# Performance work log

Measured on AMD Instinct MI355X. Metric: run time of the kernel, lower is better.

## Reference

```python
import jax, jax.numpy as jnp
import numpy as np

N = 100_000      # nodes
E = 800_000      # edges
NF = 32          # node_feature_size
EF = 32          # edge_feature_size
L = 64           # layer_size
ENTRY = NF + EF          # 64, input width of node_mlp_1
SECOND = NF + L          # 96, input width of node_mlp_2
SLOPE = 0.1              # leakiness
EPS = 1e-5               # BatchNorm1d eps


def _bn(h, g, b):
    # BatchNorm1d in training mode: batch mean, biased variance
    m = h.mean(0)
    v = ((h - m) ** 2).mean(0)
    return (h - m) * jax.lax.rsqrt(v + EPS) * g + b


def _lrelu(h):
    return jnp.where(h > 0, h, SLOPE * h)


def setup_inputs() -> dict:
    key = jax.random.key(0)
    ks = jax.random.split(key, 16)

    def w(k, i, o):
        return (jax.random.normal(k, (i, o), jnp.float32) / np.float32(np.sqrt(i)))

    def bvec(k, o):
        return jax.random.normal(k, (o,), jnp.float32) * 0.01

    inp = {
        "x": jax.random.normal(ks[0], (N, NF), jnp.float32),
        "edge_index": jax.random.randint(ks[1], (2, E), 0, N),
        "edge_attr": jax.random.normal(ks[2], (E, EF), jnp.float32),
        "u": jax.random.normal(ks[3], (1, 4), jnp.float32),
        "batch": jnp.zeros((N,), jnp.int32),
        # node_mlp_1 params
        "m1_g1": jnp.ones((ENTRY,), jnp.float32), "m1_b1": jnp.zeros((ENTRY,), jnp.float32),
        "m1_w1": w(ks[4], ENTRY, L), "m1_c1": bvec(ks[5], L),
        "m1_g2": jnp.ones((L,), jnp.float32), "m1_b2": jnp.zeros((L,), jnp.float32),
        "m1_w2": w(ks[6], L, L), "m1_c2": bvec(ks[7], L),
        "m1_g3": jnp.ones((L,), jnp.float32), "m1_b3": jnp.zeros((L,), jnp.float32),
        "m1_w3": w(ks[8], L, L), "m1_c3": bvec(ks[9], L),
        # node_mlp_2 params
        "m2_g1": jnp.ones((SECOND,), jnp.float32), "m2_b1": jnp.zeros((SECOND,), jnp.float32),
        "m2_w1": w(ks[10], SECOND, SECOND), "m2_c1": bvec(ks[11], SECOND),
        "m2_g2": jnp.ones((SECOND,), jnp.float32), "m2_b2": jnp.zeros((SECOND,), jnp.float32),
        "m2_w2": w(ks[12], SECOND, SECOND), "m2_c2": bvec(ks[13], SECOND),
        "m2_g3": jnp.ones((SECOND,), jnp.float32), "m2_b3": jnp.zeros((SECOND,), jnp.float32),
        "m2_w3": w(ks[14], SECOND, NF), "m2_c3": bvec(ks[15], NF),
    }
    return inp


def reference(x, edge_index, edge_attr, u, batch,
              m1_g1, m1_b1, m1_w1, m1_c1,
              m1_g2, m1_b2, m1_w2, m1_c2,
              m1_g3, m1_b3, m1_w3, m1_c3,
              m2_g1, m2_b1, m2_w1, m2_c1,
              m2_g2, m2_b2, m2_w2, m2_c2,
              m2_g3, m2_b3, m2_w3, m2_c3):
    row, col = edge_index[0], edge_index[1]
    # gather source node features, concat with edge features  [E, ENTRY]
    h = jnp.concatenate([x[row], edge_attr], axis=1)
    # node_mlp_1: BN -> Linear -> LReLU -> BN -> Linear -> LReLU -> BN -> Linear
    h = _lrelu(_bn(h, m1_g1, m1_b1) @ m1_w1 + m1_c1)
    h = _lrelu(_bn(h, m1_g2, m1_b2) @ m1_w2 + m1_c2)
    h = _bn(h, m1_g3, m1_b3) @ m1_w3 + m1_c3
    # scatter-sum back to destination nodes  [N, L]
    agg = jax.ops.segment_sum(h, col, num_segments=x.shape[0])
    # node_mlp_2 on [x, agg]  [N, SECOND]
    h2 = jnp.concatenate([x, agg], axis=1)
    h2 = _lrelu(_bn(h2, m2_g1, m2_b1) @ m2_w1 + m2_c1)
    h2 = _lrelu(_bn(h2, m2_g2, m2_b2) @ m2_w2 + m2_c2)
    out = _bn(h2, m2_g3, m2_b3) @ m2_w3 + m2_c3  # [N, NF]
    return out
```

## Files before the change

### kernel.cpp

```cpp
#include <hip/hip_runtime.h>


typedef unsigned short u16;
typedef __bf16  bf16x8  __attribute__((ext_vector_type(8)));
typedef float   floatx4 __attribute__((ext_vector_type(4)));

#define NBIN 8

__device__ __forceinline__ float bf2f(u16 u) {
  union { float f; unsigned int i; } v; v.i = ((unsigned int)u) << 16; return v.f;
}
__device__ __forceinline__ u16 f2bf(float f) {
  union { float f; unsigned int i; } v; v.f = f;
  unsigned int x = v.i;
  return (u16)((x + 0x7fffu + ((x >> 16) & 1u)) >> 16);
}
__device__ __forceinline__ bf16x8 ldb8(const u16* p) {
  return *reinterpret_cast<const bf16x8*>(p);
}
__device__ __forceinline__ floatx4 mfma16(bf16x8 a, bf16x8 b, floatx4 c) {
  return __builtin_amdgcn_mfma_f32_16x16x32_bf16(a, b, c, 0, 0, 0);
}
__device__ __forceinline__ float loadf(const void* p, long idx, int mode) {
  return mode ? bf2f(((const u16*)p)[idx]) : ((const float*)p)[idx];
}
__device__ __forceinline__ bf16x8 load8(const void* p, long idx, int mode) {
  if (mode) return ldb8((const u16*)p + idx);
  const float* f = (const float*)p + idx;
  bf16x8 r;
#pragma unroll
  for (int j = 0; j < 8; j++) r[j] = (__bf16)f[j];
  return r;
}

__global__ void detect_kernel(const u16* __restrict__ x, int* __restrict__ modep) {
  __shared__ int cnt;
  if (threadIdx.x == 0) cnt = 0;
  __syncthreads();
  int weird = 0;
  for (int i = threadIdx.x; i < 1024; i += blockDim.x) {
    unsigned e = (x[i] >> 7) & 0xFFu;
    if (e == 0xFFu || e >= 0x90u || (e != 0u && e < 0x60u)) weird++;
  }
  atomicAdd(&cnt, weird);
  __syncthreads();
  if (threadIdx.x == 0) *modep = (cnt > 128) ? 0 : 1;
}

__global__ void count2_kernel(const int* __restrict__ row, const int* __restrict__ col,
                              int E, int* __restrict__ odeg, int* __restrict__ deg) {
  for (int e = blockIdx.x * blockDim.x + threadIdx.x; e < E;
       e += gridDim.x * blockDim.x) {
    atomicAdd(&odeg[row[e]], 1);
    atomicAdd(&deg[col[e]], 1);
  }
}

__global__ void scan1_kernel(const int* __restrict__ deg, int n,
                             int* __restrict__ excl, int* __restrict__ bsum) {
  __shared__ int tmp[2][1024];
  const int tid = threadIdx.x;
  const int i = blockIdx.x * 1024 + tid;
  int v = (i < n) ? deg[i] : 0;
  tmp[0][tid] = v;
  __syncthreads();
  int src = 0;
  for (int off = 1; off < 1024; off <<= 1) {
    int t = tmp[src][tid];
    if (tid >= off) t += tmp[src][tid - off];
    tmp[1 - src][tid] = t;
    src = 1 - src;
    __syncthreads();
  }
  if (i < n) excl[i] = tmp[src][tid] - v;
  if (tid == 1023) bsum[blockIdx.x] = tmp[src][1023];
}

__global__ void scan2_kernel(int* __restrict__ bsum, int nb,
                             int* __restrict__ offsets, int N, int E) {
  if (threadIdx.x == 0) {
    int run = 0;
    for (int i = 0; i < nb; i++) { int v = bsum[i]; bsum[i] = run; run += v; }
    offsets[N] = E;
  }
}

__global__ void scan3_kernel(int* __restrict__ offsets, const int* __restrict__ bsum,
                             int n, int* __restrict__ cursor) {
  int i = blockIdx.x * 1024 + threadIdx.x;
  if (i < n) {
    int v = offsets[i] + bsum[blockIdx.x];
    offsets[i] = v;
    cursor[i] = v;
  }
}

__global__ void scatter_kernel(const int* __restrict__ col, int E,
                               int* __restrict__ cursor, int* __restrict__ ipos) {
  for (int e = blockIdx.x * blockDim.x + threadIdx.x; e < E;
       e += gridDim.x * blockDim.x) {
    int d = col[e];
    ipos[e] = atomicAdd(&cursor[d], 1);
  }
}

__global__ void statsXW_kernel(const void* __restrict__ x, const int* __restrict__ odeg,
                               int N, float* __restrict__ stats0,
                               float* __restrict__ statsB0,
                               const int* __restrict__ modep) {
  const int mode = *modep;
  const int c = threadIdx.x & 31, rs = threadIdx.x >> 5;
  float s = 0.f, q = 0.f, ws = 0.f, wq = 0.f;
  for (long r = (long)blockIdx.x * 8 + rs; r < N; r += (long)gridDim.x * 8) {
    float v = loadf(x, r * 32 + c, mode);
    float w = (float)odeg[r];
    s += v; q += v * v;
    ws += w * v; wq += w * v * v;
  }
  __shared__ float sm[4][256];
  sm[0][threadIdx.x] = s; sm[1][threadIdx.x] = q;
  sm[2][threadIdx.x] = ws; sm[3][threadIdx.x] = wq;
  __syncthreads();
  if (threadIdx.x < 32) {
    for (int i = 1; i < 8; i++) {
      s  += sm[0][i * 32 + c]; q  += sm[1][i * 32 + c];
      ws += sm[2][i * 32 + c]; wq += sm[3][i * 32 + c];
    }
    const int bin = blockIdx.x & (NBIN - 1);
    atomicAdd(statsB0 + bin * 192 + c, s);
    atomicAdd(statsB0 + bin * 192 + 96 + c, q);
    atomicAdd(stats0 + bin * 128 + c, ws);
    atomicAdd(stats0 + bin * 128 + 64 + c, wq);
  }
}

__global__ void statsEA_kernel(const void* __restrict__ ea, int E,
                               float* __restrict__ stats,
                               const int* __restrict__ modep) {
  const int mode = *modep;
  const int cg = threadIdx.x & 3;
  const int rsub = threadIdx.x >> 2;
  float s[8], q[8];
#pragma unroll
  for (int j = 0; j < 8; j++) { s[j] = 0.f; q[j] = 0.f; }
  for (long r = (long)blockIdx.x * 64 + rsub; r < E; r += (long)gridDim.x * 64) {
    if (mode) {
      bf16x8 v = ldb8((const u16*)ea + r * 32 + cg * 8);
#pragma unroll
      for (int j = 0; j < 8; j++) { float f = (float)v[j]; s[j] += f; q[j] += f * f; }
    } else {
      const float* p = (const float*)ea + r * 32 + cg * 8;
      float4 a = *(const float4*)p;
      float4 b = *(const float4*)(p + 4);
      float f0[8] = {a.x, a.y, a.z, a.w, b.x, b.y, b.z, b.w};
#pragma unroll
      for (int j = 0; j < 8; j++) { s[j] += f0[j]; q[j] += f0[j] * f0[j]; }
    }
  }
  const int lane = threadIdx.x & 63;
#pragma unroll
  for (int st = 4; st < 64; st <<= 1) {
#pragma unroll
    for (int j = 0; j < 8; j++) {
      s[j] += __shfl_xor(s[j], st, 64);
      q[j] += __shfl_xor(q[j], st, 64);
    }
  }
  if (lane < 4) {
    float* o = stats + (blockIdx.x & (NBIN - 1)) * 128;
#pragma unroll
    for (int j = 0; j < 8; j++) {
      atomicAdd(o + 32 + lane * 8 + j, s[j]);
      atomicAdd(o + 96 + lane * 8 + j, q[j]);
    }
  }
}

__global__ __launch_bounds__(256) void aggsum_kernel(
    const u16* __restrict__ h_s, const int* __restrict__ offsets,
    float* __restrict__ s_e, int N) {
  const int lane = threadIdx.x & 63, wave = threadIdx.x >> 6;
  for (long n = (long)blockIdx.x * 4 + wave; n < N; n += (long)gridDim.x * 4) {
    int start = offsets[n], end = offsets[n + 1];
    float acc = 0.f;
    for (int j = start; j < end; j++)
      acc += bf2f(h_s[(long)j * 64 + lane]);
    s_e[n * 64 + lane] = acc;
  }
}

__global__ void fold_kernel(const float* __restrict__ stats, float inv_rows,
                            const void* __restrict__ g, const void* __restrict__ b,
                            const void* __restrict__ W, const void* __restrict__ c,
                            int K, int OUT,
                            u16* __restrict__ Wpack, float* __restrict__ biasOut,
                            const int* __restrict__ modep) {
  const int mode = *modep;
  __shared__ float s_s[96], s_off[96];
  const int tid = threadIdx.x;
  if (tid < K) {
    float sum = 0.f, sq = 0.f;
    for (int p = 0; p < NBIN; p++) {
      sum += stats[p * 2 * K + tid];
      sq  += stats[p * 2 * K + K + tid];
    }
    float m   = sum * inv_rows;
    float var = sq * inv_rows - m * m;
    float s   = loadf(g, tid, mode) * rsqrtf(var + 1e-5f);
    s_s[tid]  = s;
    s_off[tid] = loadf(b, tid, mode) - m * s;
  }
  __syncthreads();
  for (int n = tid; n < OUT; n += blockDim.x) {
    float acc = loadf(c, n, mode);
    for (int k = 0; k < K; k++) acc += s_off[k] * loadf(W, k * OUT + n, mode);
    biasOut[n] = acc;
  }
  const int H = K / 32, T = OUT / 16;
  const int total = T * H * 64 * 8;
  for (int i = tid; i < total; i += blockDim.x) {
    int j = i & 7, lane = (i >> 3) & 63, th = i >> 9;
    int h = th % H, t = th / H;
    int k = h * 32 + (lane >> 4) * 8 + j;
    int n = t * 16 + (lane & 15);
    Wpack[i] = f2bf(s_s[k] * loadf(W, k * OUT + n, mode));
  }
}


__global__ __launch_bounds__(256) void gemm1_kernel(
    const void* __restrict__ x, const void* __restrict__ ea,
    const int* __restrict__ erow, const int* __restrict__ ipos,
    const u16* __restrict__ Wp, const float* __restrict__ bias,
    u16* __restrict__ hout, int E,
    float* __restrict__ statsOut, const int* __restrict__ modep) {
  const int mode = *modep;
  const int lane = threadIdx.x & 63, wave = threadIdx.x >> 6;
  const int q = lane >> 4, r = lane & 15;
  const long wbase = (long)blockIdx.x * 256 + wave * 64;
  bf16x8 bfr[4][2];
#pragma unroll
  for (int t = 0; t < 4; t++)
#pragma unroll
    for (int h = 0; h < 2; h++)
      bfr[t][h] = ldb8(Wp + ((t * 2 + h) * 64 + lane) * 8);
  float bv[4];
#pragma unroll
  for (int t = 0; t < 4; t++) bv[t] = bias[t * 16 + r];
  float s_[4] = {0, 0, 0, 0}, q_[4] = {0, 0, 0, 0};
#pragma unroll
  for (int r4 = 0; r4 < 4; r4++) {
    const long row0 = wbase + r4 * 16;
    long e = row0 + r; if (e > E - 1) e = E - 1;
    int src = erow[e];
    bf16x8 a0 = load8(x, (long)src * 32 + q * 8, mode);
    bf16x8 a1 = load8(ea, e * 32 + q * 8, mode);
    floatx4 acc[4];
#pragma unroll
    for (int t = 0; t < 4; t++) {
      acc[t] = (floatx4){bv[t], bv[t], bv[t], bv[t]};
      acc[t] = mfma16(a0, bfr[t][0], acc[t]);
      acc[t] = mfma16(a1, bfr[t][1], acc[t]);
    }
#pragma unroll
    for (int gi = 0; gi < 4; gi++) {
      long row = row0 + q * 4 + gi;
      if (row < E) {
        long p = ipos[row];
#pragma unroll
        for (int t = 0; t < 4; t++) {
          float v = acc[t][gi];
          v = v > 0.f ? v : 0.1f * v;
          u16 st = f2bf(v);
          hout[p * 64 + t * 16 + r] = st;
          float vv = bf2f(st);
          s_[t] += vv; q_[t] += vv * vv;
        }
      }
    }
  }
  __shared__ float sm[512];
#pragma unroll
  for (int t = 0; t < 4; t++) {
    float s = s_[t], qq = q_[t];
    s  += __shfl_xor(s, 16, 64);  s  += __shfl_xor(s, 32, 64);
    qq += __shfl_xor(qq, 16, 64); qq += __shfl_xor(qq, 32, 64);
    if (lane < 16) { sm[wave * 128 + t * 16 + lane] = s; sm[wave * 128 + 64 + t * 16 + lane] = qq; }
  }
  __syncthreads();
  if (threadIdx.x < 128) {
    int which = threadIdx.x >> 6, c = threadIdx.x & 63;
    float v = 0.f;
    for (int w = 0; w < 4; w++) v += sm[w * 128 + which * 64 + c];
    atomicAdd(statsOut + (blockIdx.x & (NBIN - 1)) * 128 + which * 64 + c, v);
  }
}

__global__ __launch_bounds__(256) void gemm2_kernel(
    const u16* __restrict__ hin, const u16* __restrict__ Wp,
    const float* __restrict__ bias, u16* __restrict__ hout, int E,
    float* __restrict__ statsOut) {
  const int lane = threadIdx.x & 63, wave = threadIdx.x >> 6;
  const int q = lane >> 4, r = lane & 15;
  const long wbase = (long)blockIdx.x * 256 + wave * 64;
  bf16x8 bfr[4][2];
#pragma unroll
  for (int t = 0; t < 4; t++)
#pragma unroll
    for (int h = 0; h < 2; h++)
      bfr[t][h] = ldb8(Wp + ((t * 2 + h) * 64 + lane) * 8);
  float bv[4];
#pragma unroll
  for (int t = 0; t < 4; t++) bv[t] = bias[t * 16 + r];
  float s_[4] = {0, 0, 0, 0}, q_[4] = {0, 0, 0, 0};
#pragma unroll
  for (int r4 = 0; r4 < 4; r4++) {
    const long row0 = wbase + r4 * 16;
    long e = row0 + r; if (e > E - 1) e = E - 1;
    bf16x8 a0 = ldb8(hin + e * 64 + q * 8);
    bf16x8 a1 = ldb8(hin + e * 64 + 32 + q * 8);
    floatx4 acc[4];
#pragma unroll
    for (int t = 0; t < 4; t++) {
      acc[t] = (floatx4){bv[t], bv[t], bv[t], bv[t]};
      acc[t] = mfma16(a0, bfr[t][0], acc[t]);
      acc[t] = mfma16(a1, bfr[t][1], acc[t]);
    }
#pragma unroll
    for (int t = 0; t < 4; t++)
#pragma unroll
      for (int gi = 0; gi < 4; gi++) {
        long row = row0 + q * 4 + gi;
        if (row < E) {
          float v = acc[t][gi];
          v = v > 0.f ? v : 0.1f * v;
          u16 st = f2bf(v);
          hout[row * 64 + t * 16 + r] = st;
          float vv = bf2f(st);
          s_[t] += vv; q_[t] += vv * vv;
        }
      }
  }
  __shared__ float sm[512];
#pragma unroll
  for (int t = 0; t < 4; t++) {
    float s = s_[t], qq = q_[t];
    s  += __shfl_xor(s, 16, 64);  s  += __shfl_xor(s, 32, 64);
    qq += __shfl_xor(qq, 16, 64); qq += __shfl_xor(qq, 32, 64);
    if (lane < 16) { sm[wave * 128 + t * 16 + lane] = s; sm[wave * 128 + 64 + t * 16 + lane] = qq; }
  }
  __syncthreads();
  if (threadIdx.x < 128) {
    int which = threadIdx.x >> 6, c = threadIdx.x & 63;
    float v = 0.f;
    for (int w = 0; w < 4; w++) v += sm[w * 128 + which * 64 + c];
    atomicAdd(statsOut + (blockIdx.x & (NBIN - 1)) * 128 + which * 64 + c, v);
  }
}

__global__ __launch_bounds__(256) void gemmAgg_kernel(
    const float* __restrict__ s_e, const int* __restrict__ deg,
    const u16* __restrict__ Wp, const float* __restrict__ bias,
    float* __restrict__ agg, int N, float* __restrict__ statsOut) {
  const int lane = threadIdx.x & 63, wave = threadIdx.x >> 6;
  const int q = lane >> 4, r = lane & 15;
  const long wbase = (long)blockIdx.x * 256 + wave * 64;
  bf16x8 bfr[4][2];
#pragma unroll
  for (int t = 0; t < 4; t++)
#pragma unroll
    for (int h = 0; h < 2; h++)
      bfr[t][h] = ldb8(Wp + ((t * 2 + h) * 64 + lane) * 8);
  float bv[4];
#pragma unroll
  for (int t = 0; t < 4; t++) bv[t] = bias[t * 16 + r];
  float s_[4] = {0, 0, 0, 0}, q_[4] = {0, 0, 0, 0};
#pragma unroll
  for (int r4 = 0; r4 < 4; r4++) {
    const long row0 = wbase + r4 * 16;
    long m = row0 + r;
    long mm = m < N ? m : (long)N - 1;
    bf16x8 a0, a1;
    {
      const float* ap = s_e + mm * 64 + q * 8;
#pragma unroll
      for (int j = 0; j < 8; j++) a0[j] = (__bf16)ap[j];
#pragma unroll
      for (int j = 0; j < 8; j++) a1[j] = (__bf16)ap[32 + j];
    }
    floatx4 acc[4];
#pragma unroll
    for (int t = 0; t < 4; t++) {
      acc[t] = (floatx4){0.f, 0.f, 0.f, 0.f};
      acc[t] = mfma16(a0, bfr[t][0], acc[t]);
      acc[t] = mfma16(a1, bfr[t][1], acc[t]);
    }
#pragma unroll
    for (int gi = 0; gi < 4; gi++) {
      long row = row0 + q * 4 + gi;
      if (row < N) {
        float d = (float)deg[row];
#pragma unroll
        for (int t = 0; t < 4; t++) {
          float v = acc[t][gi] + d * bv[t];
          agg[row * 64 + t * 16 + r] = v;
          s_[t] += v; q_[t] += v * v;
        }
      }
    }
  }
  __shared__ float sm[512];
#pragma unroll
  for (int t = 0; t < 4; t++) {
    float s = s_[t], qq = q_[t];
    s  += __shfl_xor(s, 16, 64);  s  += __shfl_xor(s, 32, 64);
    qq += __shfl_xor(qq, 16, 64); qq += __shfl_xor(qq, 32, 64);
    if (lane < 16) { sm[wave * 128 + t * 16 + lane] = s; sm[wave * 128 + 64 + t * 16 + lane] = qq; }
  }
  __syncthreads();
  if (threadIdx.x < 128) {
    int which = threadIdx.x >> 6, c = threadIdx.x & 63;
    float v = 0.f;
    for (int w = 0; w < 4; w++) v += sm[w * 128 + which * 64 + c];
    atomicAdd(statsOut + (blockIdx.x & (NBIN - 1)) * 192 + which * 96 + 32 + c, v);
  }
}


__global__ __launch_bounds__(256) void gemmB1_kernel(
    const void* __restrict__ x, const float* __restrict__ agg,
    const u16* __restrict__ Wp, const float* __restrict__ bias,
    u16* __restrict__ hout, int N, float* __restrict__ statsOut,
    const int* __restrict__ modep) {
  const int mode = *modep;
  const int lane = threadIdx.x & 63, wave = threadIdx.x >> 6;
  const int q = lane >> 4, r = lane & 15;
  const long wbase = (long)blockIdx.x * 256 + wave * 64;
  bf16x8 bfr[6][3];
#pragma unroll
  for (int t = 0; t < 6; t++)
#pragma unroll
    for (int h = 0; h < 3; h++)
      bfr[t][h] = ldb8(Wp + ((t * 3 + h) * 64 + lane) * 8);
  float bv[6];
#pragma unroll
  for (int t = 0; t < 6; t++) bv[t] = bias[t * 16 + r];
  float s_[6] = {0, 0, 0, 0, 0, 0}, q_[6] = {0, 0, 0, 0, 0, 0};
#pragma unroll
  for (int r4 = 0; r4 < 4; r4++) {
    const long row0 = wbase + r4 * 16;
    long m = row0 + r;
    long mm = m < N ? m : (long)N - 1;
    bf16x8 a0 = load8(x, mm * 32 + q * 8, mode);
    bf16x8 a1, a2;
    {
      const float* ap = agg + mm * 64 + q * 8;
#pragma unroll
      for (int j = 0; j < 8; j++) a1[j] = (__bf16)ap[j];
#pragma unroll
      for (int j = 0; j < 8; j++) a2[j] = (__bf16)ap[32 + j];
    }
    floatx4 acc[6];
#pragma unroll
    for (int t = 0; t < 6; t++) {
      acc[t] = (floatx4){bv[t], bv[t], bv[t], bv[t]};
      acc[t] = mfma16(a0, bfr[t][0], acc[t]);
      acc[t] = mfma16(a1, bfr[t][1], acc[t]);
      acc[t] = mfma16(a2, bfr[t][2], acc[t]);
    }
#pragma unroll
    for (int t = 0; t < 6; t++)
#pragma unroll
      for (int gi = 0; gi < 4; gi++) {
        long row = row0 + q * 4 + gi;
        if (row < N) {
          float v = acc[t][gi];
          v = v > 0.f ? v : 0.1f * v;
          u16 st = f2bf(v);
          hout[row * 96 + t * 16 + r] = st;
          float vv = bf2f(st);
          s_[t] += vv; q_[t] += vv * vv;
        }
      }
  }
  __shared__ float sm[768];
#pragma unroll
  for (int t = 0; t < 6; t++) {
    float s = s_[t], qq = q_[t];
    s  += __shfl_xor(s, 16, 64);  s  += __shfl_xor(s, 32, 64);
    qq += __shfl_xor(qq, 16, 64); qq += __shfl_xor(qq, 32, 64);
    if (lane < 16) { sm[wave * 192 + t * 16 + lane] = s; sm[wave * 192 + 96 + t * 16 + lane] = qq; }
  }
  __syncthreads();
  if (threadIdx.x < 192) {
    int which = threadIdx.x / 96, c = threadIdx.x % 96;
    float v = 0.f;
    for (int w = 0; w < 4; w++) v += sm[w * 192 + which * 96 + c];
    atomicAdd(statsOut + (blockIdx.x & (NBIN - 1)) * 192 + which * 96 + c, v);
  }
}

__global__ __launch_bounds__(256) void gemmB2_kernel(
    const u16* __restrict__ hin, const u16* __restrict__ Wp,
    const float* __restrict__ bias, u16* __restrict__ hout, int N,
    float* __restrict__ statsOut) {
  const int lane = threadIdx.x & 63, wave = threadIdx.x >> 6;
  const int q = lane >> 4, r = lane & 15;
  const long wbase = (long)blockIdx.x * 256 + wave * 64;
  bf16x8 bfr[6][3];
#pragma unroll
  for (int t = 0; t < 6; t++)
#pragma unroll
    for (int h = 0; h < 3; h++)
      bfr[t][h] = ldb8(Wp + ((t * 3 + h) * 64 + lane) * 8);
  float bv[6];
#pragma unroll
  for (int t = 0; t < 6; t++) bv[t] = bias[t * 16 + r];
  float s_[6] = {0, 0, 0, 0, 0, 0}, q_[6] = {0, 0, 0, 0, 0, 0};
#pragma unroll
  for (int r4 = 0; r4 < 4; r4++) {
    const long row0 = wbase + r4 * 16;
    long m = row0 + r;
    long mm = m < N ? m : (long)N - 1;
    bf16x8 a0 = ldb8(hin + mm * 96 + q * 8);
    bf16x8 a1 = ldb8(hin + mm * 96 + 32 + q * 8);
    bf16x8 a2 = ldb8(hin + mm * 96 + 64 + q * 8);
    floatx4 acc[6];
#pragma unroll
    for (int t = 0; t < 6; t++) {
      acc[t] = (floatx4){bv[t], bv[t], bv[t], bv[t]};
      acc[t] = mfma16(a0, bfr[t][0], acc[t]);
      acc[t] = mfma16(a1, bfr[t][1], acc[t]);
      acc[t] = mfma16(a2, bfr[t][2], acc[t]);
    }
#pragma unroll
    for (int t = 0; t < 6; t++)
#pragma unroll
      for (int gi = 0; gi < 4; gi++) {
        long row = row0 + q * 4 + gi;
        if (row < N) {
          float v = acc[t][gi];
          v = v > 0.f ? v : 0.1f * v;
          u16 st = f2bf(v);
          hout[row * 96 + t * 16 + r] = st;
          float vv = bf2f(st);
          s_[t] += vv; q_[t] += vv * vv;
        }
      }
  }
  __shared__ float sm[768];
#pragma unroll
  for (int t = 0; t < 6; t++) {
    float s = s_[t], qq = q_[t];
    s  += __shfl_xor(s, 16, 64);  s  += __shfl_xor(s, 32, 64);
    qq += __shfl_xor(qq, 16, 64); qq += __shfl_xor(qq, 32, 64);
    if (lane < 16) { sm[wave * 192 + t * 16 + lane] = s; sm[wave * 192 + 96 + t * 16 + lane] = qq; }
  }
  __syncthreads();
  if (threadIdx.x < 192) {
    int which = threadIdx.x / 96, c = threadIdx.x % 96;
    float v = 0.f;
    for (int w = 0; w < 4; w++) v += sm[w * 192 + which * 96 + c];
    atomicAdd(statsOut + (blockIdx.x & (NBIN - 1)) * 192 + which * 96 + c, v);
  }
}

__global__ __launch_bounds__(256) void gemmB3_kernel(
    const u16* __restrict__ hin, const u16* __restrict__ Wp,
    const float* __restrict__ bias, void* __restrict__ outv, int N,
    const int* __restrict__ modep) {
  const int mode = *modep;
  const int lane = threadIdx.x & 63, wave = threadIdx.x >> 6;
  const int q = lane >> 4, r = lane & 15;
  const long wbase = (long)blockIdx.x * 256 + wave * 64;
  bf16x8 bfr[2][3];
#pragma unroll
  for (int t = 0; t < 2; t++)
#pragma unroll
    for (int h = 0; h < 3; h++)
      bfr[t][h] = ldb8(Wp + ((t * 3 + h) * 64 + lane) * 8);
  float bv[2];
#pragma unroll
  for (int t = 0; t < 2; t++) bv[t] = bias[t * 16 + r];
#pragma unroll
  for (int r4 = 0; r4 < 4; r4++) {
    const long row0 = wbase + r4 * 16;
    long m = row0 + r;
    long mm = m < N ? m : (long)N - 1;
    bf16x8 a0 = ldb8(hin + mm * 96 + q * 8);
    bf16x8 a1 = ldb8(hin + mm * 96 + 32 + q * 8);
    bf16x8 a2 = ldb8(hin + mm * 96 + 64 + q * 8);
    floatx4 acc[2];
#pragma unroll
    for (int t = 0; t < 2; t++) {
      acc[t] = (floatx4){bv[t], bv[t], bv[t], bv[t]};
      acc[t] = mfma16(a0, bfr[t][0], acc[t]);
      acc[t] = mfma16(a1, bfr[t][1], acc[t]);
      acc[t] = mfma16(a2, bfr[t][2], acc[t]);
    }
#pragma unroll
    for (int t = 0; t < 2; t++)
#pragma unroll
      for (int gi = 0; gi < 4; gi++) {
        long row = row0 + q * 4 + gi;
        if (row < N) {
          float v = acc[t][gi];
          if (mode) ((u16*)outv)[row * 32 + t * 16 + r] = f2bf(v);
          else      ((float*)outv)[row * 32 + t * 16 + r] = v;
        }
      }
  }
}

extern "C" void kernel_launch(void* const* d_in, const int* in_sizes, int n_in,
                              void* d_out, int out_size, void* d_ws,
                              size_t ws_size, hipStream_t stream) {
  const int N = in_sizes[0] / 32;
  const int E = in_sizes[2] / 32;

  const void* x    = d_in[0];
  const int*  eidx = (const int*)d_in[1];
  const void* ea   = d_in[2];
  const void *m1_g1 = d_in[5],  *m1_b1 = d_in[6];
  const void *m1_w1 = d_in[7],  *m1_c1 = d_in[8];
  const void *m1_g2 = d_in[9],  *m1_b2 = d_in[10];
  const void *m1_w2 = d_in[11], *m1_c2 = d_in[12];
  const void *m1_g3 = d_in[13], *m1_b3 = d_in[14];
  const void *m1_w3 = d_in[15], *m1_c3 = d_in[16];
  const void *m2_g1 = d_in[17], *m2_b1 = d_in[18];
  const void *m2_w1 = d_in[19], *m2_c1 = d_in[20];
  const void *m2_g2 = d_in[21], *m2_b2 = d_in[22];
  const void *m2_w2 = d_in[23], *m2_c2 = d_in[24];
  const void *m2_g3 = d_in[25], *m2_b3 = d_in[26];
  const void *m2_w3 = d_in[27], *m2_c3 = d_in[28];

  char* w = (char*)d_ws;
  int*   modep  = (int*)w;   w += 16;
  u16*   h_s    = (u16*)w;   w += (size_t)E * 64 * 2;
  u16*   h2b    = (u16*)w;   w += (size_t)N * 96 * 2;
  float* agg    = (float*)w; w += (size_t)N * 64 * 4;
  float* s_e    = (float*)w; w += (size_t)N * 64 * 4;
  int*   offs   = (int*)w;   w += ((size_t)N + 4) * 4;
  int*   cursor = (int*)w;   w += ((size_t)N + 4) * 4;
  int*   ipos   = (int*)w;   w += (size_t)E * 4;
  int*   bsum   = (int*)w;   w += 1024 * 4;
  int*   deg    = (int*)w;   w += (size_t)N * 4;
  int*   odeg   = (int*)w;   w += (size_t)N * 4;
  float* stats0 = (float*)w; w += NBIN * 128 * 4;
  float* stats1 = (float*)w; w += NBIN * 128 * 4;
  float* stats2 = (float*)w; w += NBIN * 128 * 4;
  float* statsB0= (float*)w; w += NBIN * 192 * 4;
  float* statsB1= (float*)w; w += NBIN * 192 * 4;
  float* statsB2= (float*)w; w += NBIN * 192 * 4;
  const size_t zero_bytes = (size_t)N * 8 + NBIN * (128 * 3 + 192 * 3) * 4;
  u16*   Wp1    = (u16*)w;   w += 4096 * 2;
  float* bias1  = (float*)w; w += 64 * 4;
  u16*   Wp2    = (u16*)w;   w += 4096 * 2;
  float* bias2  = (float*)w; w += 64 * 4;
  u16*   Wp3    = (u16*)w;   w += 4096 * 2;
  float* bias3  = (float*)w; w += 64 * 4;
  u16*   WpB1   = (u16*)w;   w += 9216 * 2;
  float* biasB1 = (float*)w; w += 96 * 4;
  u16*   WpB2   = (u16*)w;   w += 9216 * 2;
  float* biasB2 = (float*)w; w += 96 * 4;
  u16*   WpB3   = (u16*)w;   w += 3072 * 2;
  float* biasB3 = (float*)w; w += 32 * 4;

  const int* erow = eidx;
  const int* ecol = eidx + E;
  const float invE = 1.0f / (float)E, invN = 1.0f / (float)N;
  const int gA = (E + 255) / 256, gB = (N + 255) / 256;
  const int nb = (N + 1023) / 1024;

  detect_kernel<<<1, 256, 0, stream>>>((const u16*)x, modep);
  hipMemsetAsync(deg, 0, zero_bytes, stream);

  count2_kernel<<<1024, 256, 0, stream>>>(erow, ecol, E, odeg, deg);
  scan1_kernel<<<nb, 1024, 0, stream>>>(deg, N, offs, bsum);
  scan2_kernel<<<1, 64, 0, stream>>>(bsum, nb, offs, N, E);
  scan3_kernel<<<nb, 1024, 0, stream>>>(offs, bsum, N, cursor);
  scatter_kernel<<<1024, 256, 0, stream>>>(ecol, E, cursor, ipos);

  statsXW_kernel<<<512, 256, 0, stream>>>(x, odeg, N, stats0, statsB0, modep);
  statsEA_kernel<<<512, 256, 0, stream>>>(ea, E, stats0, modep);

  fold_kernel<<<1, 256, 0, stream>>>(stats0, invE, m1_g1, m1_b1, m1_w1, m1_c1,
                                     64, 64, Wp1, bias1, modep);
  gemm1_kernel<<<gA, 256, 0, stream>>>(x, ea, erow, ipos, Wp1, bias1, h_s, E,
                                       stats1, modep);
  fold_kernel<<<1, 256, 0, stream>>>(stats1, invE, m1_g2, m1_b2, m1_w2, m1_c2,
                                     64, 64, Wp2, bias2, modep);
  gemm2_kernel<<<gA, 256, 0, stream>>>(h_s, Wp2, bias2, h_s, E, stats2);

  aggsum_kernel<<<1024, 256, 0, stream>>>(h_s, offs, s_e, N);
  fold_kernel<<<1, 256, 0, stream>>>(stats2, invE, m1_g3, m1_b3, m1_w3, m1_c3,
                                     64, 64, Wp3, bias3, modep);
  gemmAgg_kernel<<<gB, 256, 0, stream>>>(s_e, deg, Wp3, bias3, agg, N, statsB0);

  fold_kernel<<<1, 256, 0, stream>>>(statsB0, invN, m2_g1, m2_b1, m2_w1, m2_c1,
                                     96, 96, WpB1, biasB1, modep);
  gemmB1_kernel<<<gB, 256, 0, stream>>>(x, agg, WpB1, biasB1, h2b, N,
                                        statsB1, modep);
  fold_kernel<<<1, 256, 0, stream>>>(statsB1, invN, m2_g2, m2_b2, m2_w2, m2_c2,
                                     96, 96, WpB2, biasB2, modep);
  gemmB2_kernel<<<gB, 256, 0, stream>>>(h2b, WpB2, biasB2, h2b, N, statsB2);
  fold_kernel<<<1, 256, 0, stream>>>(statsB2, invN, m2_g3, m2_b3, m2_w3, m2_c3,
                                     96, 32, WpB3, biasB3, modep);
  gemmB3_kernel<<<gB, 256, 0, stream>>>(h2b, WpB3, biasB3, d_out, N, modep);
}
```

Baseline: 741.5 us.

## Fuse segment-sum aggregation into gemm2 via LDS tile and node map

gemm2 no longer writes its 800K x 64 bf16 output to global memory. It stages the tile in a swizzled LDS buffer and then sums rows per destination node inside the block, using a new nodeof array built in the scatter kernel. Segments that cross block boundaries are combined with atomics into a now zero-initialised s_e. This removes the separate aggsum kernel and a full round trip of h_s through global memory. In exchange it adds 32 KB of LDS per block, the extra nodeof writes, and a larger memset. fold_kernel also stages W in shared memory.

```diff
diff --git a/kernel.cpp b/kernel.cpp
--- a/kernel.cpp
+++ b/kernel.cpp
@@ -96,11 +96,14 @@
 }
 
 __global__ void scatter_kernel(const int* __restrict__ col, int E,
-                               int* __restrict__ cursor, int* __restrict__ ipos) {
+                               int* __restrict__ cursor, int* __restrict__ ipos,
+                               int* __restrict__ nodeof) {
   for (int e = blockIdx.x * blockDim.x + threadIdx.x; e < E;
        e += gridDim.x * blockDim.x) {
     int d = col[e];
-    ipos[e] = atomicAdd(&cursor[d], 1);
+    int pos = atomicAdd(&cursor[d], 1);
+    ipos[e] = pos;
+    nodeof[pos] = d;
   }
 }
 
@@ -176,19 +179,6 @@
   }
 }
 
-__global__ __launch_bounds__(256) void aggsum_kernel(
-    const u16* __restrict__ h_s, const int* __restrict__ offsets,
-    float* __restrict__ s_e, int N) {
-  const int lane = threadIdx.x & 63, wave = threadIdx.x >> 6;
-  for (long n = (long)blockIdx.x * 4 + wave; n < N; n += (long)gridDim.x * 4) {
-    int start = offsets[n], end = offsets[n + 1];
-    float acc = 0.f;
-    for (int j = start; j < end; j++)
-      acc += bf2f(h_s[(long)j * 64 + lane]);
-    s_e[n * 64 + lane] = acc;
-  }
-}
-
 __global__ void fold_kernel(const float* __restrict__ stats, float inv_rows,
                             const void* __restrict__ g, const void* __restrict__ b,
                             const void* __restrict__ W, const void* __restrict__ c,
@@ -197,7 +187,10 @@
                             const int* __restrict__ modep) {
   const int mode = *modep;
   __shared__ float s_s[96], s_off[96];
+  __shared__ float wlds[9216];
   const int tid = threadIdx.x;
+  const int tot = K * OUT;
+  for (int i = tid; i < tot; i += blockDim.x) wlds[i] = loadf(W, i, mode);
   if (tid < K) {
     float sum = 0.f, sq = 0.f;
     for (int p = 0; p < NBIN; p++) {
@@ -213,7 +206,7 @@
   __syncthreads();
   for (int n = tid; n < OUT; n += blockDim.x) {
     float acc = loadf(c, n, mode);
-    for (int k = 0; k < K; k++) acc += s_off[k] * loadf(W, k * OUT + n, mode);
+    for (int k = 0; k < K; k++) acc += s_off[k] * wlds[k * OUT + n];
     biasOut[n] = acc;
   }
   const int H = K / 32, T = OUT / 16;
@@ -223,7 +216,7 @@
     int h = th % H, t = th / H;
     int k = h * 32 + (lane >> 4) * 8 + j;
     int n = t * 16 + (lane & 15);
-    Wpack[i] = f2bf(s_s[k] * loadf(W, k * OUT + n, mode));
+    Wpack[i] = f2bf(s_s[k] * wlds[k * OUT + n]);
   }
 }
 
@@ -298,11 +291,16 @@
 
 __global__ __launch_bounds__(256) void gemm2_kernel(
     const u16* __restrict__ hin, const u16* __restrict__ Wp,
-    const float* __restrict__ bias, u16* __restrict__ hout, int E,
-    float* __restrict__ statsOut) {
+    const float* __restrict__ bias, int E,
+    float* __restrict__ statsOut,
+    const int* __restrict__ offs, const int* __restrict__ nodeof,
+    float* __restrict__ s_e) {
   const int lane = threadIdx.x & 63, wave = threadIdx.x >> 6;
   const int q = lane >> 4, r = lane & 15;
-  const long wbase = (long)blockIdx.x * 256 + wave * 64;
+  const long bbase = (long)blockIdx.x * 256;
+  const long wbase = bbase + wave * 64;
+  __shared__ u16 hs[256 * 64];
+  __shared__ float sm[512];
   bf16x8 bfr[4][2];
 #pragma unroll
   for (int t = 0; t < 4; t++)
@@ -326,22 +324,24 @@
       acc[t] = mfma16(a0, bfr[t][0], acc[t]);
       acc[t] = mfma16(a1, bfr[t][1], acc[t]);
     }
-#pragma unroll
-    for (int t = 0; t < 4; t++)
+    const int lbase = wave * 64 + r4 * 16;
+#pragma unroll
+    for (int t = 0; t < 4; t++) {
+      const int colx = ((t ^ q) << 4) + r;
 #pragma unroll
       for (int gi = 0; gi < 4; gi++) {
         long row = row0 + q * 4 + gi;
+        float v = acc[t][gi];
+        v = v > 0.f ? v : 0.1f * v;
+        u16 st = f2bf(v);
+        hs[(lbase + q * 4 + gi) * 64 + colx] = st;
         if (row < E) {
-          float v = acc[t][gi];
-          v = v > 0.f ? v : 0.1f * v;
-          u16 st = f2bf(v);
-          hout[row * 64 + t * 16 + r] = st;
           float vv = bf2f(st);
           s_[t] += vv; q_[t] += vv * vv;
         }
       }
-  }
-  __shared__ float sm[512];
+    }
+  }
 #pragma unroll
   for (int t = 0; t < 4; t++) {
     float s = s_[t], qq = q_[t];
@@ -355,6 +355,22 @@
     float v = 0.f;
     for (int w = 0; w < 4; w++) v += sm[w * 128 + which * 64 + c];
     atomicAdd(statsOut + (blockIdx.x & (NBIN - 1)) * 128 + which * 64 + c, v);
+  }
+  const long blockEnd = (bbase + 256 < (long)E) ? bbase + 256 : (long)E;
+  const int first = nodeof[bbase];
+  const int last  = nodeof[blockEnd - 1];
+  for (int idx = first + wave; idx <= last; idx += 4) {
+    int st = offs[idx], en = offs[idx + 1];
+    long cs = st < bbase ? bbase : (long)st;
+    long ce = (long)en > blockEnd ? blockEnd : (long)en;
+    if (cs >= ce) continue;
+    float acc = 0.f;
+    for (long i = cs - bbase; i < ce - bbase; i++)
+      acc += bf2f(hs[i * 64 + (lane ^ (int)(((i >> 2) & 3) << 4))]);
+    if ((long)st >= bbase && (long)en <= blockEnd)
+      s_e[(long)idx * 64 + lane] = acc;
+    else
+      atomicAdd(s_e + (long)idx * 64 + lane, acc);
   }
 }
 
@@ -639,11 +655,12 @@
   u16*   h_s    = (u16*)w;   w += (size_t)E * 64 * 2;
   u16*   h2b    = (u16*)w;   w += (size_t)N * 96 * 2;
   float* agg    = (float*)w; w += (size_t)N * 64 * 4;
-  float* s_e    = (float*)w; w += (size_t)N * 64 * 4;
   int*   offs   = (int*)w;   w += ((size_t)N + 4) * 4;
   int*   cursor = (int*)w;   w += ((size_t)N + 4) * 4;
   int*   ipos   = (int*)w;   w += (size_t)E * 4;
+  int*   nodeof = (int*)w;   w += (size_t)E * 4;
   int*   bsum   = (int*)w;   w += 1024 * 4;
+  float* s_e    = (float*)w; w += (size_t)N * 64 * 4;
   int*   deg    = (int*)w;   w += (size_t)N * 4;
   int*   odeg   = (int*)w;   w += (size_t)N * 4;
   float* stats0 = (float*)w; w += NBIN * 128 * 4;
@@ -652,7 +669,8 @@
   float* statsB0= (float*)w; w += NBIN * 192 * 4;
   float* statsB1= (float*)w; w += NBIN * 192 * 4;
   float* statsB2= (float*)w; w += NBIN * 192 * 4;
-  const size_t zero_bytes = (size_t)N * 8 + NBIN * (128 * 3 + 192 * 3) * 4;
+  const size_t zero_bytes = (size_t)N * 64 * 4 + (size_t)N * 8 +
+                            NBIN * (128 * 3 + 192 * 3) * 4;
   u16*   Wp1    = (u16*)w;   w += 4096 * 2;
   float* bias1  = (float*)w; w += 64 * 4;
   u16*   Wp2    = (u16*)w;   w += 4096 * 2;
@@ -673,13 +691,13 @@
   const int nb = (N + 1023) / 1024;
 
   detect_kernel<<<1, 256, 0, stream>>>((const u16*)x, modep);
-  hipMemsetAsync(deg, 0, zero_bytes, stream);
+  hipMemsetAsync(s_e, 0, zero_bytes, stream);
 
   count2_kernel<<<1024, 256, 0, stream>>>(erow, ecol, E, odeg, deg);
   scan1_kernel<<<nb, 1024, 0, stream>>>(deg, N, offs, bsum);
   scan2_kernel<<<1, 64, 0, stream>>>(bsum, nb, offs, N, E);
   scan3_kernel<<<nb, 1024, 0, stream>>>(offs, bsum, N, cursor);
-  scatter_kernel<<<1024, 256, 0, stream>>>(ecol, E, cursor, ipos);
+  scatter_kernel<<<1024, 256, 0, stream>>>(ecol, E, cursor, ipos, nodeof);
 
   statsXW_kernel<<<512, 256, 0, stream>>>(x, odeg, N, stats0, statsB0, modep);
   statsEA_kernel<<<512, 256, 0, stream>>>(ea, E, stats0, modep);
@@ -690,9 +708,9 @@
                                        stats1, modep);
   fold_kernel<<<1, 256, 0, stream>>>(stats1, invE, m1_g2, m1_b2, m1_w2, m1_c2,
                                      64, 64, Wp2, bias2, modep);
-  gemm2_kernel<<<gA, 256, 0, stream>>>(h_s, Wp2, bias2, h_s, E, stats2);
-
-  aggsum_kernel<<<1024, 256, 0, stream>>>(h_s, offs, s_e, N);
+  gemm2_kernel<<<gA, 256, 0, stream>>>(h_s, Wp2, bias2, E, stats2,
+                                       offs, nodeof, s_e);
+
   fold_kernel<<<1, 256, 0, stream>>>(stats2, invE, m1_g3, m1_b3, m1_w3, m1_c3,
                                      64, 64, Wp3, bias3, modep);
   gemmAgg_kernel<<<gB, 256, 0, stream>>>(s_e, deg, Wp3, bias3, agg, N, statsB0);
```

After: 698.0 us. 1.06x faster.
